# Kernel tuning notes

Hardware: AMD Instinct MI355X
Metric: run time of the kernel (lower is better)

Reference implementation:

```python
import jax, jax.numpy as jnp
import numpy as np
import math

B = 64
N = 2048
EMBED_DIM = 128
N_HEADS = 8
VAL_DIM = EMBED_DIM // N_HEADS  # 16
KEY_DIM = VAL_DIM               # key_dim defaults to val_dim
CLIP = True
NORM = 1.0 / math.sqrt(KEY_DIM)


def _uniform_param(k, shape):
    # torch init: uniform(-stdv, stdv) with stdv = 1/sqrt(size(-1))
    stdv = 1.0 / math.sqrt(shape[-1])
    return jax.random.uniform(k, shape, jnp.float32, -stdv, stdv)


def setup_inputs() -> dict:
    key = jax.random.key(0)
    ks = jax.random.split(key, 11)
    h = jax.random.normal(ks[0], (B, N, EMBED_DIM), jnp.float32)
    adj_c = jax.random.randint(ks[1], (B, N, N), 0, 2).astype(jnp.float32)
    phone_set = jax.random.randint(ks[2], (B,), 1, N - 1)
    return dict(
        h=h, adj_c=adj_c, phone_set=phone_set,
        Wq_bf=_uniform_param(ks[3], (EMBED_DIM, KEY_DIM)),
        Wk_bf=_uniform_param(ks[4], (EMBED_DIM, KEY_DIM)),
        Wv_bf=_uniform_param(ks[5], (EMBED_DIM, VAL_DIM)),
        Wo_bf=_uniform_param(ks[6], (VAL_DIM, EMBED_DIM)),
        Wq_af=_uniform_param(ks[7], (EMBED_DIM, KEY_DIM)),
        Wk_af=_uniform_param(ks[8], (EMBED_DIM, KEY_DIM)),
        Wv_af=_uniform_param(ks[9], (EMBED_DIM, VAL_DIM)),
        Wo_af=_uniform_param(ks[10], (VAL_DIM, EMBED_DIM)),
    )


def _attend(h, h_phone, adj_row, pos_mask, Wq, Wk, Wv, Wo):
    # h: (B,N,D), h_phone: (B,D), adj_row: (B,N), pos_mask: (B,N) bool
    Q = h_phone @ Wq                              # (B,K)
    K = jnp.einsum('bnd,dk->bnk', h, Wk)          # (B,N,K)
    V = jnp.einsum('bnd,dk->bnk', h, Wv)          # (B,N,V)
    compat = NORM * jnp.einsum('bk,bnk->bn', Q, K)
    if CLIP:
        compat = 10.0 * jnp.tanh(compat)
    valid = pos_mask & (adj_row != 0)
    # masked stable softmax over valid positions; fully-masked rows -> zeros
    mx = jnp.max(jnp.where(valid, compat, -jnp.inf), axis=-1, keepdims=True)
    mx = jnp.where(jnp.isfinite(mx), mx, 0.0)
    e = jnp.where(valid, jnp.exp(compat - mx), 0.0)
    s = jnp.sum(e, axis=-1, keepdims=True)
    attn = (e / jnp.where(s > 0, s, 1.0)) * adj_row   # matches attn * adj slice
    head = jnp.einsum('bn,bnk->bk', attn, V)          # (B,V)
    return head @ Wo                                  # (B,D)


def reference(h, adj_c, phone_set, Wq_bf, Wk_bf, Wv_bf, Wo_bf,
              Wq_af, Wk_af, Wv_af, Wo_af):
    b, n, d = h.shape
    bidx = jnp.arange(b)
    h_phone = h[bidx, phone_set]        # (B,D) single query per graph
    adj_row = adj_c[bidx, phone_set]    # (B,N) adjacency row of phone node
    pos = jnp.arange(n)[None, :]
    mask_bf = pos < phone_set[:, None]   # indices [0, phone)
    mask_af = pos >= phone_set[:, None]  # indices [phone, N)
    g_bf = _attend(h, h_phone, adj_row, mask_bf, Wq_bf, Wk_bf, Wv_bf, Wo_bf)
    g_af = _attend(h, h_phone, adj_row, mask_af, Wq_af, Wk_af, Wv_af, Wo_af)
    return (g_bf, g_af)
```

## Files before the change

kernel.cpp:

```cpp
#include <hip/hip_runtime.h>
#include <math.h>

#define BB 64
#define NN 2048
#define DD 128
#define KD 16
#define NORMF 0.25f
#define CHUNK 32
#define PSTRIDE 260

__device__ __forceinline__ void wave_lds_fence() {
    asm volatile("s_waitcnt lgkmcnt(0)" ::: "memory");
    __builtin_amdgcn_wave_barrier();
}

template <int P>
__global__ __launch_bounds__(256, 2)
void attn_main(const float* __restrict__ h,
               const float* __restrict__ adj,
               const int*   __restrict__ phone,
               const float* __restrict__ Wq_bf, const float* __restrict__ Wk_bf,
               const float* __restrict__ Wq_af, const float* __restrict__ Wk_af,
               float* __restrict__ ws)
{
    constexpr int K = 16 / P;
    const int tid  = threadIdx.x;
    const int wid  = tid >> 6;
    const int lane = tid & 63;
    const int half = lane >> 5;
    const int l    = lane & 31;
    const int dbase = 4 * l;

    const int xcd  = blockIdx.x & 7;
    const int slot = blockIdx.x >> 3;
    const int b    = xcd + 8 * (slot / P);
    const int bip  = slot % P;
    const int ph   = phone[b];

    __shared__ float hp[DD];
    __shared__ float qpart[32][8];
    __shared__ float q[2][KD];
    __shared__ float w_s[2][DD];
    __shared__ float part[4][CHUNK][33];
    __shared__ float ea_s[4][CHUNK];
    __shared__ float red_h[4][2][DD];
    __shared__ float red_s[4][2];

    const float* hb     = h + (size_t)b * NN * DD;
    const float* adjrow = adj + ((size_t)b * NN + ph) * NN;
    const int chbase    = (bip * 4 + wid) * K;

    float adjv[K];
    #pragma unroll
    for (int c = 0; c < K; ++c) adjv[c] = adjrow[(chbase + c) * CHUNK + l];

    if (tid < DD) hp[tid] = hb[(size_t)ph * DD + tid];

    const int pair = tid >> 3, sub = tid & 7;
    const int brq = pair >> 4, kq = pair & 15;
    const float* Wq = brq ? Wq_af : Wq_bf;
    float wqr[16];
    #pragma unroll
    for (int i = 0; i < 16; ++i) wqr[i] = Wq[(sub * 16 + i) * KD + kq];

    const int brw = tid >> 7, dw = tid & 127;
    const float* Wk = brw ? Wk_af : Wk_bf;
    float wkr[KD];
    #pragma unroll
    for (int k = 0; k < KD; ++k) wkr[k] = Wk[dw * KD + k];

    auto load_chunk = [&](float4* hv, unsigned long long mask, int n0) {
        #pragma unroll
        for (int t = 0; t < 16; ++t) {
            const int r = 2 * t + half;
            hv[t] = make_float4(0.f, 0.f, 0.f, 0.f);
            if ((mask >> r) & 1ull)
                hv[t] = *(const float4*)(hb + (size_t)(n0 + r) * DD + dbase);
        }
    };

    float4 hv0[16], hv1[16];
    {
        const unsigned long long m0 = __ballot(adjv[0] != 0.f);
        load_chunk(hv0, m0, (chbase + 0) * CHUNK);
        if (K > 1) {
            const unsigned long long m1 = __ballot(adjv[1] != 0.f);
            load_chunk(hv1, m1, (chbase + 1) * CHUNK);
        }
    }

    __syncthreads();
    {
        float acc = 0.f;
        #pragma unroll
        for (int i = 0; i < 16; ++i) acc += hp[sub * 16 + i] * wqr[i];
        qpart[pair][sub] = acc;
    }
    __syncthreads();
    if (tid < 32) {
        float acc = 0.f;
        #pragma unroll
        for (int i = 0; i < 8; ++i) acc += qpart[tid][i];
        q[tid >> 4][tid & 15] = acc;
    }
    __syncthreads();
    {
        float acc = 0.f;
        #pragma unroll
        for (int k = 0; k < KD; ++k) acc += wkr[k] * q[brw][k];
        w_s[brw][dw] = NORMF * acc;
    }
    __syncthreads();

    const float4 wbf = *(const float4*)(&w_s[0][dbase]);
    const float4 waf = *(const float4*)(&w_s[1][dbase]);

    float sbf = 0.f, saf = 0.f;
    float hgbf[4] = {0, 0, 0, 0}, hgaf[4] = {0, 0, 0, 0};

    auto compute_chunk = [&](int n0, const float4* hv, float adjc) {
        #pragma unroll
        for (int t = 0; t < 16; ++t) {
            const int r = 2 * t + half;
            const float4 w = ((n0 + r) >= ph) ? waf : wbf;
            part[wid][r][l] = hv[t].x * w.x + hv[t].y * w.y + hv[t].z * w.z + hv[t].w * w.w;
        }
        wave_lds_fence();

        float a0 = 0.f, a1 = 0.f, a2 = 0.f, a3 = 0.f;
        #pragma unroll
        for (int j = 0; j < 32; j += 4) {
            a0 += part[wid][l][j];
            a1 += part[wid][l][j + 1];
            a2 += part[wid][l][j + 2];
            a3 += part[wid][l][j + 3];
        }
        const float p = (a0 + a1) + (a2 + a3);
        const float e = __expf(10.f * tanhf(p) - 10.f);
        const float es = (adjc != 0.f) ? e : 0.f;
        const float ea = es * adjc;
        const bool rowaf = (n0 + l) >= ph;
        sbf += rowaf ? 0.f : es;
        saf += rowaf ? es : 0.f;
        if (lane < 32) ea_s[wid][l] = ea;
        wave_lds_fence();

        #pragma unroll
        for (int t = 0; t < 16; ++t) {
            const int r = 2 * t + half;
            const float ear = ea_s[wid][r];
            const bool af = (n0 + r) >= ph;
            const float eb = af ? 0.f : ear;
            const float ef = af ? ear : 0.f;
            hgbf[0] += eb * hv[t].x; hgbf[1] += eb * hv[t].y;
            hgbf[2] += eb * hv[t].z; hgbf[3] += eb * hv[t].w;
            hgaf[0] += ef * hv[t].x; hgaf[1] += ef * hv[t].y;
            hgaf[2] += ef * hv[t].z; hgaf[3] += ef * hv[t].w;
        }
    };

    compute_chunk((chbase + 0) * CHUNK, hv0, adjv[0]);
    if (K > 1) compute_chunk((chbase + 1) * CHUNK, hv1, adjv[1]);

    #pragma unroll
    for (int cc = 2; cc < K; cc += 2) {
        const unsigned long long m0 = __ballot(adjv[cc] != 0.f);
        load_chunk(hv0, m0, (chbase + cc) * CHUNK);
        if (cc + 1 < K) {
            const unsigned long long m1 = __ballot(adjv[cc + 1] != 0.f);
            load_chunk(hv1, m1, (chbase + cc + 1) * CHUNK);
        }
        compute_chunk((chbase + cc) * CHUNK, hv0, adjv[cc]);
        if (cc + 1 < K) compute_chunk((chbase + cc + 1) * CHUNK, hv1, adjv[cc + 1]);
    }

    #pragma unroll
    for (int m = 1; m <= 16; m <<= 1) {
        sbf += __shfl_xor(sbf, m, 64);
        saf += __shfl_xor(saf, m, 64);
    }
    #pragma unroll
    for (int i = 0; i < 4; ++i) {
        hgbf[i] += __shfl_xor(hgbf[i], 32, 64);
        hgaf[i] += __shfl_xor(hgaf[i], 32, 64);
    }
    if (lane < 32) {
        #pragma unroll
        for (int i = 0; i < 4; ++i) {
            red_h[wid][0][dbase + i] = hgbf[i];
            red_h[wid][1][dbase + i] = hgaf[i];
        }
    }
    if (lane == 0) { red_s[wid][0] = sbf; red_s[wid][1] = saf; }
    __syncthreads();

    {
        const int br = tid >> 7, d = tid & 127;
        float* op = ws + (size_t)(b * P + bip) * PSTRIDE;
        op[br * DD + d] = red_h[0][br][d] + red_h[1][br][d] + red_h[2][br][d] + red_h[3][br][d];
        if (tid < 2)
            op[2 * DD + tid] = red_s[0][tid] + red_s[1][tid] + red_s[2][tid] + red_s[3][tid];
    }
}

template <int P>
__global__ __launch_bounds__(256)
void finalize_kernel(const float* __restrict__ Wv_bf, const float* __restrict__ Wo_bf,
                     const float* __restrict__ Wv_af, const float* __restrict__ Wo_af,
                     const float* __restrict__ ws, float* __restrict__ out)
{
    const int b = blockIdx.x;
    const int tid = threadIdx.x;
    __shared__ float hs[2][DD];
    __shared__ float ssum[2];
    __shared__ float hpart[32][8];
    __shared__ float head[2][KD];

    const int pair = tid >> 3, sub = tid & 7;
    const int brv = pair >> 4, kv = pair & 15;
    const float* Wv = brv ? Wv_af : Wv_bf;
    float wvr[16];
    #pragma unroll
    for (int i = 0; i < 16; ++i) wvr[i] = Wv[(sub * 16 + i) * KD + kv];

    const int br2 = tid >> 7, j = tid & 127;
    const float* Wo = br2 ? Wo_af : Wo_bf;
    float wor[KD];
    #pragma unroll
    for (int k = 0; k < KD; ++k) wor[k] = Wo[k * DD + j];

    const float* base = ws + (size_t)b * P * PSTRIDE;
    {
        float acc = 0.f;
        #pragma unroll
        for (int p = 0; p < P; ++p) acc += base[(size_t)p * PSTRIDE + br2 * DD + j];
        hs[br2][j] = acc;
    }
    if (tid < 2) {
        float acc = 0.f;
        #pragma unroll
        for (int p = 0; p < P; ++p) acc += base[(size_t)p * PSTRIDE + 2 * DD + tid];
        ssum[tid] = acc;
    }
    __syncthreads();

    {
        float acc = 0.f;
        #pragma unroll
        for (int i = 0; i < 16; ++i) acc += hs[brv][sub * 16 + i] * wvr[i];
        hpart[pair][sub] = acc;
    }
    __syncthreads();
    if (tid < 32) {
        float acc = 0.f;
        #pragma unroll
        for (int i = 0; i < 8; ++i) acc += hpart[tid][i];
        head[tid >> 4][tid & 15] = acc;
    }
    __syncthreads();

    {
        const float s = ssum[br2];
        const float inv = (s > 0.f) ? 1.f / s : 0.f;
        float acc = 0.f;
        #pragma unroll
        for (int k = 0; k < KD; ++k) acc += head[br2][k] * wor[k];
        out[br2 * BB * DD + b * DD + j] = acc * inv;
    }
}

extern "C" void kernel_launch(void* const* d_in, const int* in_sizes, int n_in,
                              void* d_out, int out_size, void* d_ws, size_t ws_size,
                              hipStream_t stream) {
    const float* h     = (const float*)d_in[0];
    const float* adj   = (const float*)d_in[1];
    const int*   phone = (const int*)d_in[2];
    const float* Wq_bf = (const float*)d_in[3];
    const float* Wk_bf = (const float*)d_in[4];
    const float* Wv_bf = (const float*)d_in[5];
    const float* Wo_bf = (const float*)d_in[6];
    const float* Wq_af = (const float*)d_in[7];
    const float* Wk_af = (const float*)d_in[8];
    const float* Wv_af = (const float*)d_in[9];
    const float* Wo_af = (const float*)d_in[10];

    float* out = (float*)d_out;
    float* ws  = (float*)d_ws;

    int P = 8;
    while (P > 1 && (size_t)BB * P * PSTRIDE * sizeof(float) > ws_size) P >>= 1;

    switch (P) {
    case 8:
        attn_main<8><<<BB * 8, 256, 0, stream>>>(h, adj, phone, Wq_bf, Wk_bf, Wq_af, Wk_af, ws);
        finalize_kernel<8><<<BB, 256, 0, stream>>>(Wv_bf, Wo_bf, Wv_af, Wo_af, ws, out);
        break;
    case 4:
        attn_main<4><<<BB * 4, 256, 0, stream>>>(h, adj, phone, Wq_bf, Wk_bf, Wq_af, Wk_af, ws);
        finalize_kernel<4><<<BB, 256, 0, stream>>>(Wv_bf, Wo_bf, Wv_af, Wo_af, ws, out);
        break;
    case 2:
        attn_main<2><<<BB * 2, 256, 0, stream>>>(h, adj, phone, Wq_bf, Wk_bf, Wq_af, Wk_af, ws);
        finalize_kernel<2><<<BB, 256, 0, stream>>>(Wv_bf, Wo_bf, Wv_af, Wo_af, ws, out);
        break;
    default:
        attn_main<1><<<BB, 256, 0, stream>>>(h, adj, phone, Wq_bf, Wk_bf, Wq_af, Wk_af, ws);
        finalize_kernel<1><<<BB, 256, 0, stream>>>(Wv_bf, Wo_bf, Wv_af, Wo_af, ws, out);
        break;
    }
}
```

Measured before the change: 17.51 us.

## Split work across more blocks, raise occupancy, and specialize uniform chunks

Raises the per-batch block split from 8 to 16, so each wave handles a single 32-row chunk, and raises the launch bound to 4 blocks per CU. The Wq/Wk register preloads and the second chunk buffer are dropped to cut register pressure. Chunks lying entirely before or after the phone index take a branch-free path with one accumulator set. The exp(10*tanh(p)-10) is rewritten as exp2/rcp intrinsics. In exchange, software double-buffering of loads is lost and the workspace and finalize reduction double in size.

```diff
diff --git a/kernel.cpp b/kernel.cpp
--- a/kernel.cpp
+++ b/kernel.cpp
@@ -8,6 +8,7 @@
 #define NORMF 0.25f
 #define CHUNK 32
 #define PSTRIDE 260
+#define LOG2E 1.4426950408889634f
 
 __device__ __forceinline__ void wave_lds_fence() {
     asm volatile("s_waitcnt lgkmcnt(0)" ::: "memory");
@@ -15,7 +16,7 @@
 }
 
 template <int P>
-__global__ __launch_bounds__(256, 2)
+__global__ __launch_bounds__(256, 4)
 void attn_main(const float* __restrict__ h,
                const float* __restrict__ adj,
                const int*   __restrict__ phone,
@@ -56,19 +57,6 @@
 
     if (tid < DD) hp[tid] = hb[(size_t)ph * DD + tid];
 
-    const int pair = tid >> 3, sub = tid & 7;
-    const int brq = pair >> 4, kq = pair & 15;
-    const float* Wq = brq ? Wq_af : Wq_bf;
-    float wqr[16];
-    #pragma unroll
-    for (int i = 0; i < 16; ++i) wqr[i] = Wq[(sub * 16 + i) * KD + kq];
-
-    const int brw = tid >> 7, dw = tid & 127;
-    const float* Wk = brw ? Wk_af : Wk_bf;
-    float wkr[KD];
-    #pragma unroll
-    for (int k = 0; k < KD; ++k) wkr[k] = Wk[dw * KD + k];
-
     auto load_chunk = [&](float4* hv, unsigned long long mask, int n0) {
         #pragma unroll
         for (int t = 0; t < 16; ++t) {
@@ -79,21 +67,23 @@
         }
     };
 
-    float4 hv0[16], hv1[16];
-    {
-        const unsigned long long m0 = __ballot(adjv[0] != 0.f);
-        load_chunk(hv0, m0, (chbase + 0) * CHUNK);
-        if (K > 1) {
-            const unsigned long long m1 = __ballot(adjv[1] != 0.f);
-            load_chunk(hv1, m1, (chbase + 1) * CHUNK);
-        }
-    }
-
-    __syncthreads();
-    {
-        float acc = 0.f;
-        #pragma unroll
-        for (int i = 0; i < 16; ++i) acc += hp[sub * 16 + i] * wqr[i];
+    float4 hv0[16];
+    unsigned long long m0 = __ballot(adjv[0] != 0.f);
+    load_chunk(hv0, m0, (chbase + 0) * CHUNK);
+
+    const int pair = tid >> 3, sub = tid & 7;
+    const int brq = pair >> 4, kq = pair & 15;
+    const int brw = tid >> 7, dw = tid & 127;
+
+    __syncthreads();
+    {
+        const float* Wq = brq ? Wq_af : Wq_bf;
+        float acc = 0.f;
+        #pragma unroll
+        for (int i = 0; i < 16; ++i) {
+            const int d = sub * 16 + i;
+            acc += hp[d] * Wq[d * KD + kq];
+        }
         qpart[pair][sub] = acc;
     }
     __syncthreads();
@@ -105,9 +95,10 @@
     }
     __syncthreads();
     {
-        float acc = 0.f;
-        #pragma unroll
-        for (int k = 0; k < KD; ++k) acc += wkr[k] * q[brw][k];
+        const float* Wk = brw ? Wk_af : Wk_bf;
+        float acc = 0.f;
+        #pragma unroll
+        for (int k = 0; k < KD; ++k) acc += Wk[dw * KD + k] * q[brw][k];
         w_s[brw][dw] = NORMF * acc;
     }
     __syncthreads();
@@ -118,12 +109,30 @@
     float sbf = 0.f, saf = 0.f;
     float hgbf[4] = {0, 0, 0, 0}, hgaf[4] = {0, 0, 0, 0};
 
+    auto softexp = [](float p) {
+        const float t = __builtin_amdgcn_exp2f(2.f * LOG2E * p);
+        return __builtin_amdgcn_exp2f(-20.f * LOG2E * __builtin_amdgcn_rcpf(t + 1.f));
+    };
+
     auto compute_chunk = [&](int n0, const float4* hv, float adjc) {
-        #pragma unroll
-        for (int t = 0; t < 16; ++t) {
-            const int r = 2 * t + half;
-            const float4 w = ((n0 + r) >= ph) ? waf : wbf;
-            part[wid][r][l] = hv[t].x * w.x + hv[t].y * w.y + hv[t].z * w.z + hv[t].w * w.w;
+        const bool all_bf = (n0 + CHUNK) <= ph;
+        const bool all_af = n0 >= ph;
+        const bool uniform = all_bf | all_af;
+
+        if (uniform) {
+            const float4 w = all_af ? waf : wbf;
+            #pragma unroll
+            for (int t = 0; t < 16; ++t) {
+                const int r = 2 * t + half;
+                part[wid][r][l] = hv[t].x * w.x + hv[t].y * w.y + hv[t].z * w.z + hv[t].w * w.w;
+            }
+        } else {
+            #pragma unroll
+            for (int t = 0; t < 16; ++t) {
+                const int r = 2 * t + half;
+                const float4 w = ((n0 + r) >= ph) ? waf : wbf;
+                part[wid][r][l] = hv[t].x * w.x + hv[t].y * w.y + hv[t].z * w.z + hv[t].w * w.w;
+            }
         }
         wave_lds_fence();
 
@@ -136,42 +145,54 @@
             a3 += part[wid][l][j + 3];
         }
         const float p = (a0 + a1) + (a2 + a3);
-        const float e = __expf(10.f * tanhf(p) - 10.f);
+        const float e = softexp(p);
         const float es = (adjc != 0.f) ? e : 0.f;
         const float ea = es * adjc;
-        const bool rowaf = (n0 + l) >= ph;
-        sbf += rowaf ? 0.f : es;
-        saf += rowaf ? es : 0.f;
         if (lane < 32) ea_s[wid][l] = ea;
+
+        if (uniform) {
+            if (all_af) saf += es; else sbf += es;
+        } else {
+            const bool rowaf = (n0 + l) >= ph;
+            sbf += rowaf ? 0.f : es;
+            saf += rowaf ? es : 0.f;
+        }
         wave_lds_fence();
 
-        #pragma unroll
-        for (int t = 0; t < 16; ++t) {
-            const int r = 2 * t + half;
-            const float ear = ea_s[wid][r];
-            const bool af = (n0 + r) >= ph;
-            const float eb = af ? 0.f : ear;
-            const float ef = af ? ear : 0.f;
-            hgbf[0] += eb * hv[t].x; hgbf[1] += eb * hv[t].y;
-            hgbf[2] += eb * hv[t].z; hgbf[3] += eb * hv[t].w;
-            hgaf[0] += ef * hv[t].x; hgaf[1] += ef * hv[t].y;
-            hgaf[2] += ef * hv[t].z; hgaf[3] += ef * hv[t].w;
+        if (uniform) {
+            float hg0 = 0.f, hg1 = 0.f, hg2 = 0.f, hg3 = 0.f;
+            #pragma unroll
+            for (int t = 0; t < 16; ++t) {
+                const int r = 2 * t + half;
+                const float ear = ea_s[wid][r];
+                hg0 += ear * hv[t].x; hg1 += ear * hv[t].y;
+                hg2 += ear * hv[t].z; hg3 += ear * hv[t].w;
+            }
+            if (all_af) { hgaf[0] += hg0; hgaf[1] += hg1; hgaf[2] += hg2; hgaf[3] += hg3; }
+            else        { hgbf[0] += hg0; hgbf[1] += hg1; hgbf[2] += hg2; hgbf[3] += hg3; }
+        } else {
+            #pragma unroll
+            for (int t = 0; t < 16; ++t) {
+                const int r = 2 * t + half;
+                const float ear = ea_s[wid][r];
+                const bool af = (n0 + r) >= ph;
+                const float eb = af ? 0.f : ear;
+                const float ef = af ? ear : 0.f;
+                hgbf[0] += eb * hv[t].x; hgbf[1] += eb * hv[t].y;
+                hgbf[2] += eb * hv[t].z; hgbf[3] += eb * hv[t].w;
+                hgaf[0] += ef * hv[t].x; hgaf[1] += ef * hv[t].y;
+                hgaf[2] += ef * hv[t].z; hgaf[3] += ef * hv[t].w;
+            }
         }
     };
 
     compute_chunk((chbase + 0) * CHUNK, hv0, adjv[0]);
-    if (K > 1) compute_chunk((chbase + 1) * CHUNK, hv1, adjv[1]);
-
-    #pragma unroll
-    for (int cc = 2; cc < K; cc += 2) {
-        const unsigned long long m0 = __ballot(adjv[cc] != 0.f);
-        load_chunk(hv0, m0, (chbase + cc) * CHUNK);
-        if (cc + 1 < K) {
-            const unsigned long long m1 = __ballot(adjv[cc + 1] != 0.f);
-            load_chunk(hv1, m1, (chbase + cc + 1) * CHUNK);
-        }
+
+    #pragma unroll
+    for (int cc = 1; cc < K; ++cc) {
+        const unsigned long long mc = __ballot(adjv[cc] != 0.f);
+        load_chunk(hv0, mc, (chbase + cc) * CHUNK);
         compute_chunk((chbase + cc) * CHUNK, hv0, adjv[cc]);
-        if (cc + 1 < K) compute_chunk((chbase + cc + 1) * CHUNK, hv1, adjv[cc + 1]);
     }
 
     #pragma unroll
@@ -287,10 +308,14 @@
     float* out = (float*)d_out;
     float* ws  = (float*)d_ws;
 
-    int P = 8;
+    int P = 16;
     while (P > 1 && (size_t)BB * P * PSTRIDE * sizeof(float) > ws_size) P >>= 1;
 
     switch (P) {
+    case 16:
+        attn_main<16><<<BB * 16, 256, 0, stream>>>(h, adj, phone, Wq_bf, Wk_bf, Wq_af, Wk_af, ws);
+        finalize_kernel<16><<<BB, 256, 0, stream>>>(Wv_bf, Wo_bf, Wv_af, Wo_af, ws, out);
+        break;
     case 8:
         attn_main<8><<<BB * 8, 256, 0, stream>>>(h, adj, phone, Wq_bf, Wk_bf, Wq_af, Wk_af, ws);
         finalize_kernel<8><<<BB, 256, 0, stream>>>(Wv_bf, Wo_bf, Wv_af, Wo_af, ws, out);
```

Result: slower. 31.86 us (+82.0%).
